# Optimization experiments

Measured on AMD Instinct MI355X. Metric: run time of the kernel, lower is better.

Reference implementation:

```python
import jax, jax.numpy as jnp
import numpy as np

M_NUMS = 4096
D_NUMS = 4096
PROJ = 256
EPS = 1e-10


def _lin(x, W, b):
    # torch nn.Linear: y = x @ W.T + b
    return x @ W.T + b


def setup_inputs() -> dict:
    key = jax.random.key(0)
    ks = jax.random.split(key, 16)
    N = M_NUMS + D_NUMS
    inp = {}
    inp["m_d_feat"] = jax.random.normal(ks[0], (N, PROJ), dtype=jnp.float32)
    inp["bigraph"] = jax.random.uniform(ks[1], (N, N), dtype=jnp.float32)
    # sparse-ish binary co-occurrence matrices (values !=0 / ==0 drive masks)
    inp["m_co"] = (jax.random.uniform(ks[2], (M_NUMS, M_NUMS)) < 0.1).astype(jnp.float32)
    inp["d_co"] = (jax.random.uniform(ks[3], (D_NUMS, D_NUMS)) < 0.1).astype(jnp.float32)
    # positive degrees in [1, 50) to keep 1/sqrt and 1/deg well-conditioned
    inp["m_co_deg"] = jax.random.uniform(ks[4], (M_NUMS, 2)) * 49.0 + 1.0
    inp["d_co_deg"] = jax.random.uniform(ks[5], (D_NUMS, 2)) * 49.0 + 1.0
    inp["m_d_degree"] = jax.random.uniform(ks[6], (M_NUMS,)) * 49.0 + 1.0
    inp["d_m_degree"] = jax.random.uniform(ks[7], (D_NUMS,)) * 49.0 + 1.0
    s = 0.02
    inp["Wm"] = jax.random.normal(ks[8], (3, PROJ, PROJ), dtype=jnp.float32) * s
    inp["bm"] = jnp.zeros((3, PROJ), dtype=jnp.float32)
    inp["Wd"] = jax.random.normal(ks[9], (3, PROJ, PROJ), dtype=jnp.float32) * s
    inp["bd"] = jnp.zeros((3, PROJ), dtype=jnp.float32)
    inp["Wx"] = jax.random.normal(ks[10], (8, PROJ, PROJ), dtype=jnp.float32) * s
    inp["bx"] = jnp.zeros((8, PROJ), dtype=jnp.float32)
    inp["central_m"] = jax.random.randint(ks[11], (M_NUMS,), 0, 2, dtype=jnp.int32)
    inp["central_d"] = jax.random.randint(ks[12], (D_NUMS,), 0, 2, dtype=jnp.int32)
    inp["m_nums"] = M_NUMS
    return inp


def _homog_block(feat, co, deg, W, b):
    # self-loop + degree-normalized co-occurrence / non-co-occurrence GEMMs
    n = feat.shape[0]
    diag = jnp.eye(n, dtype=bool)
    co_mask = (~diag) & (co != 0)
    non_mask = (~diag) & (co == 0)
    out = _lin(feat, W[0], b[0])  # self loop
    d0 = deg[:, 0]
    coeff0 = (1.0 / jnp.sqrt(d0[:, None] * d0[None, :] + EPS)) * co_mask.astype(feat.dtype)
    out = out + coeff0 @ _lin(feat, W[1], b[1])
    d1 = deg[:, 1]
    coeff1 = (1.0 / jnp.sqrt(d1[:, None] * d1[None, :] + EPS)) * non_mask.astype(feat.dtype)
    out = out + coeff1 @ _lin(feat, W[2], b[2])
    return out


def _cross_block(assoc, row_central, col_central, norm_row, src_feat, Wx, bx, pairs):
    # sum of 4 (central/normal x central/normal) masked-association GEMMs
    rc = row_central != 0
    cc = col_central != 0
    masks = [
        rc[:, None] & cc[None, :],
        rc[:, None] & (~cc)[None, :],
        (~rc)[:, None] & cc[None, :],
        (~rc)[:, None] & (~cc)[None, :],
    ]
    norm = (1.0 / norm_row)[:, None]
    out = jnp.zeros((assoc.shape[0], src_feat.shape[1]), dtype=src_feat.dtype)
    for mask, (i, j) in zip(masks, pairs):
        transformed = _lin(src_feat, Wx[i], bx[i]) + _lin(src_feat, Wx[j], bx[j])
        out = out + 0.5 * norm * ((assoc * mask.astype(assoc.dtype)) @ transformed)
    return out


def reference(m_d_feat, bigraph, m_co, m_co_deg, d_co, d_co_deg, m_d_degree,
              d_m_degree, Wm, bm, Wd, bd, Wx, bx, central_m, central_d, m_nums):
    m = m_nums
    m_feat = m_d_feat[:m]
    d_feat = m_d_feat[m:]

    out_m = _homog_block(m_feat, m_co, m_co_deg, Wm, bm)
    out_d = _homog_block(d_feat, d_co, d_co_deg, Wd, bd)

    # m <- d aggregation: Wx indices 0..7 =
    # [cm2cd, cd2cm, cm2nd, cd2nm, nm2cd, nd2cm, nm2nd, nd2nm]
    assoc_md = bigraph[:m, m:]
    out_m = out_m + _cross_block(assoc_md, central_m, central_d, m_d_degree,
                                 d_feat, Wx, bx,
                                 pairs=[(0, 1), (2, 5), (4, 3), (6, 7)])
    # d <- m aggregation (roles swapped)
    assoc_dm = bigraph[m:, :m]
    out_d = out_d + _cross_block(assoc_dm, central_d, central_m, d_m_degree,
                                 m_feat, Wx, bx,
                                 pairs=[(1, 0), (3, 4), (5, 2), (7, 6)])

    return jnp.concatenate([out_m, out_d], axis=0)
```

## Files before the change

kernel.cpp:

```cpp
#include <hip/hip_runtime.h>
#include <hip/hip_bf16.h>


typedef __bf16 bf16x8 __attribute__((ext_vector_type(8)));
typedef float floatx4 __attribute__((ext_vector_type(4)));
typedef float f32x4 __attribute__((ext_vector_type(4)));
using bf16 = __hip_bfloat16;

#define LDK 72

__device__ __forceinline__ float b2f(bf16 x){ return __bfloat162float(x); }
__device__ __forceinline__ bf16 f2b(float f){ return __float2bfloat16(f); }
__device__ __forceinline__ float rawb2f(unsigned short u){
  unsigned int x = ((unsigned int)u) << 16; float f; __builtin_memcpy(&f,&x,4); return f;
}
__device__ __forceinline__ unsigned short f2bu(float f){
  bf16 h = __float2bfloat16(f); unsigned short u; __builtin_memcpy(&u,&h,2); return u;
}
__device__ __forceinline__ uint4 cvt8(float4 a, float4 b){
  unsigned short u[8] = {f2bu(a.x),f2bu(a.y),f2bu(a.z),f2bu(a.w),
                         f2bu(b.x),f2bu(b.y),f2bu(b.z),f2bu(b.w)};
  uint4 v; __builtin_memcpy(&v,u,16); return v;
}
__device__ __forceinline__ void async_ld16(const void* gp, void* lp){
  typedef __attribute__((address_space(1))) const unsigned int GU;
  typedef __attribute__((address_space(3))) unsigned int LU;
  __builtin_amdgcn_global_load_lds((GU*)(unsigned long long)gp,
                                   (LU*)(unsigned int)(unsigned long long)lp,
                                   16, 0, 0);
}

__global__ void prep_kernel(const float* __restrict__ m_co_deg, const float* __restrict__ d_co_deg,
                            const float* __restrict__ m_d_degree, const float* __restrict__ d_m_degree,
                            const float* __restrict__ Wx, const float* __restrict__ bx,
                            float* __restrict__ scal, float* __restrict__ Sbuf, float* __restrict__ bSbuf)
{
  const int i = blockIdx.x*blockDim.x + threadIdx.x;
  if (i < 4096){
    scal[0*4096+i] = rsqrtf(m_co_deg[2*i]);
    scal[1*4096+i] = rsqrtf(m_co_deg[2*i+1]);
    scal[2*4096+i] = 0.5f / m_d_degree[i];
    scal[3*4096+i] = rsqrtf(d_co_deg[2*i]);
    scal[4*4096+i] = rsqrtf(d_co_deg[2*i+1]);
    scal[5*4096+i] = 0.5f / d_m_degree[i];
  }
  const int pa[4] = {0,2,3,6}, pb[4] = {1,5,4,7};
  if (i < 65536){
    #pragma unroll
    for (int s=0;s<4;s++)
      Sbuf[s*65536+i] = Wx[pa[s]*65536+i] + Wx[pb[s]*65536+i];
  }
  if (i < 256){
    #pragma unroll
    for (int s=0;s<4;s++)
      bSbuf[s*256+i] = bx[pa[s]*256+i] + bx[pb[s]*256+i];
  }
}

__global__ __launch_bounds__(256) void stage1_kernel(
    const float* __restrict__ feat, const float* __restrict__ Wm, const float* __restrict__ bm,
    const float* __restrict__ Wd, const float* __restrict__ bd,
    const float* __restrict__ Sbuf, const float* __restrict__ bSbuf, const float* __restrict__ scal,
    bf16* __restrict__ BHm, bf16* __restrict__ BHd,
    float* __restrict__ L0m, float* __restrict__ L0d,
    float* __restrict__ L2nm, float* __restrict__ L2nd,
    bf16* __restrict__ Tm, bf16* __restrict__ Td)
{
  __shared__ __align__(16) bf16 As[128*LDK];
  __shared__ __align__(16) bf16 Bs[128*LDK];
  const int p = blockIdx.y;
  const int side = p >> 3, widx = p & 7;
  const int bx_ = blockIdx.x;
  const bool modeT = (widx != 0 && widx != 7);
  const float* X = feat + (size_t)side*(4096*256);
  const float* Wb = side ? Wd : Wm;
  const float* W = (widx==0) ? Wb : (widx==7) ? (Wb + 2*65536)
                 : (widx<=2) ? (Wb + widx*65536) : (Sbuf + (widx-3)*65536);
  int rt, ct;
  if (!modeT){ rt = bx_>>1; ct = bx_&1; } else { rt = bx_&1; ct = bx_>>1; }
  const float* Amat = modeT ? W : X;
  const float* Bmat = modeT ? X : W;
  const int arow0 = rt*128, brow0 = ct*128;
  const int tid = threadIdx.x;
  const int lane = tid & 63, wv = tid>>6;
  const int wr = wv>>1, wc = wv&1, q = lane>>4, l15 = lane&15;

  floatx4 acc[4][4];
  #pragma unroll
  for (int i=0;i<4;i++)
    #pragma unroll
    for (int j=0;j<4;j++)
      #pragma unroll
      for (int r=0;r<4;r++) acc[i][j][r] = 0.f;

  for (int kt=0; kt<4; kt++){
    const int c0 = kt*64;
    __syncthreads();
    #pragma unroll
    for (int i=0;i<4;i++){
      const int id = tid + i*256;
      const int row = id>>3, kg = id&7;
      const float* ap = Amat + (size_t)(arow0+row)*256 + c0 + kg*8;
      const float* bp = Bmat + (size_t)(brow0+row)*256 + c0 + kg*8;
      float4 a0 = *(const float4*)ap, a1 = *(const float4*)(ap+4);
      float4 b0 = *(const float4*)bp, b1 = *(const float4*)(bp+4);
      *(uint4*)(&As[row*LDK + kg*8]) = cvt8(a0,a1);
      *(uint4*)(&Bs[row*LDK + kg*8]) = cvt8(b0,b1);
    }
    __syncthreads();
    #pragma unroll
    for (int ki=0; ki<2; ki++){
      bf16x8 af[4], bg[4];
      #pragma unroll
      for (int i=0;i<4;i++) af[i] = *(const bf16x8*)&As[(wr*64 + i*16 + l15)*LDK + ki*32 + q*8];
      #pragma unroll
      for (int j=0;j<4;j++) bg[j] = *(const bf16x8*)&Bs[(wc*64 + j*16 + l15)*LDK + ki*32 + q*8];
      #pragma unroll
      for (int i=0;i<4;i++)
        #pragma unroll
        for (int j=0;j<4;j++)
          acc[i][j] = __builtin_amdgcn_mfma_f32_16x16x32_bf16(af[i], bg[j], acc[i][j], 0,0,0);
    }
  }

  const float* bb = side ? bd : bm;
  const float* bias = (widx==0) ? bb : (widx==7) ? (bb + 512)
                    : (widx<=2) ? (bb + widx*256) : (bSbuf + (widx-3)*256);
  float* outF = nullptr; bf16* outB = nullptr; int pitch = 256; const float* scl = nullptr;
  if (widx==0){ outF = side? L0d : L0m; }
  else if (widx==7){ outF = side? L2nd : L2nm; }
  else if (widx==1){ outB = side? BHd : BHm; pitch = 4096; scl = scal + side*12288; }
  else if (widx==2){ outB = (side? BHd : BHm) + 256*4096; pitch = 4096; scl = scal + side*12288 + 4096; }
  else { outB = (side? Td : Tm) + (widx-3)*(256*4096); pitch = 4096; }

  #pragma unroll
  for (int i=0;i<4;i++){
    #pragma unroll
    for (int j=0;j<4;j++){
      const int gcol = brow0 + wc*64 + j*16 + l15;
      #pragma unroll
      for (int r=0;r<4;r++){
        const int grow = arow0 + wr*64 + i*16 + q*4 + r;
        float v = acc[i][j][r];
        const int nidx = modeT ? grow : gcol;
        v += bias[nidx];
        if (scl) v *= scl[gcol];
        if (outF) outF[(size_t)grow*pitch + gcol] = v;
        else      outB[(size_t)grow*pitch + gcol] = f2b(v);
      }
    }
  }
}

__global__ void stage2_kernel(const bf16* __restrict__ Tm, const bf16* __restrict__ Td,
                              const int* __restrict__ central_m, const int* __restrict__ central_d,
                              bf16* __restrict__ BXm, bf16* __restrict__ BXd)
{
  const int idx = blockIdx.x*blockDim.x + threadIdx.x;
  const int oside = idx >> 20;
  const int rem = idx & 1048575;
  const int n = rem >> 12;
  const int c = rem & 4095;
  const bf16* T = oside ? Tm : Td;
  const int* cen = oside ? central_m : central_d;
  bf16* B = oside ? BXd : BXm;
  const bool cc = cen[c] != 0;
  int v0i, v1i;
  if (!oside){ v0i = cc ? 2 : 3; v1i = cc ? 0 : 1; }
  else       { v0i = cc ? 1 : 3; v1i = cc ? 0 : 2; }
  const float v0 = b2f(T[(size_t)v0i*1048576 + (size_t)n*4096 + c]);
  const float v1 = b2f(T[(size_t)v1i*1048576 + (size_t)n*4096 + c]);
  B[(size_t)n*4096 + c]         = f2b(v0);
  B[(size_t)(256+n)*4096 + c]   = f2b(v1 - v0);
}

__global__ void colsum_kernel(const bf16* __restrict__ BHm, const bf16* __restrict__ BHd,
                              float* __restrict__ Scol)
{
  const int b = blockIdx.x;
  const int sd = b >> 8, n = b & 255;
  const int lane = threadIdx.x;
  const bf16* rowp = (sd ? BHd : BHm) + (size_t)(256+n)*4096;
  float s = 0.f;
  #pragma unroll
  for (int t=0;t<8;t++){
    const uint4 v = *(const uint4*)(rowp + t*512 + lane*8);
    unsigned short u[8]; __builtin_memcpy(u,&v,16);
    #pragma unroll
    for (int jj=0;jj<8;jj++) s += rawb2f(u[jj]);
  }
  #pragma unroll
  for (int off=32; off>0; off>>=1) s += __shfl_down(s, off);
  if (lane==0) Scol[sd*256 + n] = s;
}

__global__ __launch_bounds__(512,2) void gemm_kernel(
    const float* __restrict__ bigraph, const float* __restrict__ m_co, const float* __restrict__ d_co,
    const int* __restrict__ central_m, const int* __restrict__ central_d,
    const float* __restrict__ scal,
    const bf16* __restrict__ BHm, const bf16* __restrict__ BHd,
    const bf16* __restrict__ BXm, const bf16* __restrict__ BXd,
    float* __restrict__ partial)
{
  __shared__ __align__(16) bf16 As[2][128*32];
  __shared__ __align__(16) bf16 Bs[2][512*32];
  const int bid = blockIdx.x;
  const int w = (bid & 7)*32 + (bid >> 3);
  const int seg = w & 1, mt = (w >> 1) & 31, p = w >> 6;
  const int s = p & 1;
  const bool maskmode = (p < 2);
  const int k0 = seg*2048;
  const int rowbase = mt*128;
  const float* Asrc; int apitch; int acoff;
  if (p==0){ Asrc = m_co; apitch = 4096; acoff = 0; }
  else if (p==1){ Asrc = d_co; apitch = 4096; acoff = 0; }
  else if (p==2){ Asrc = bigraph; apitch = 8192; acoff = 4096; }
  else { Asrc = bigraph + (size_t)4096*8192; apitch = 8192; acoff = 0; }
  const bf16* B0 = (p==0) ? BHm : (p==1) ? BHd : (p==2) ? BXm : BXd;

  const int tid = threadIdx.x;
  const int lane = tid&63, wv = tid>>6;
  const int wr = wv>>2, wc = wv&3;
  const int q = lane>>4, l15 = lane&15;

  const int a_row = tid>>2, a_sg = tid&3;
  const int a_g  = a_sg ^ ((a_row>>1)&3);
  const int a_gr = rowbase + a_row;
  const float* a_base = Asrc + (size_t)a_gr*apitch + acoff + a_g*8;
  int b_roff[4]; int b_ldsoff[4];
  #pragma unroll
  for (int j=0;j<4;j++){
    const int cb = wv*256 + j*64;
    const int chunk = cb + lane;
    const int row = chunk>>2, sg = chunk&3;
    const int gg = sg ^ ((row>>1)&3);
    b_roff[j] = row*4096 + gg*8;
    b_ldsoff[j] = cb*8;
  }

  floatx4 acc0[4][4], acc1[4][4];
  #pragma unroll
  for (int i=0;i<4;i++)
    #pragma unroll
    for (int j=0;j<4;j++)
      #pragma unroll
      for (int r=0;r<4;r++){ acc0[i][j][r] = 0.f; acc1[i][j][r] = 0.f; }

  auto issueB = [&](int kkg, int buf){
    #pragma unroll
    for (int j=0;j<4;j++)
      async_ld16(B0 + (size_t)b_roff[j] + kkg, &Bs[buf][b_ldsoff[j]]);
  };
  auto writeA = [&](f32x4 a0, f32x4 a1, int kkg, int buf){
    const float av[8] = {a0[0],a0[1],a0[2],a0[3],a1[0],a1[1],a1[2],a1[3]};
    unsigned short u[8];
    if (maskmode){
      const int cbase = kkg + a_g*8;
      #pragma unroll
      for (int jj=0;jj<8;jj++)
        u[jj] = (av[jj]!=0.0f && (cbase+jj)!=a_gr) ? (unsigned short)0x3F80 : (unsigned short)0;
    } else {
      #pragma unroll
      for (int jj=0;jj<8;jj++) u[jj] = f2bu(av[jj]);
    }
    uint4 w4; __builtin_memcpy(&w4,u,16);
    *(uint4*)(&As[buf][tid*8]) = w4;
  };

  {
    const int kkg = k0;
    const float* ap = a_base + kkg;
    f32x4 a0 = __builtin_nontemporal_load((const f32x4*)ap);
    f32x4 a1 = __builtin_nontemporal_load((const f32x4*)(ap+4));
    issueB(kkg, 0);
    writeA(a0, a1, kkg, 0);
  }
  __syncthreads();

  for (int kt=0; kt<64; kt++){
    const int cur = kt & 1;
    const bool pre = (kt+1 < 64);
    f32x4 a0, a1;
    const int nkkg = k0 + (kt+1)*32;
    if (pre){
      const float* ap = a_base + nkkg;
      a0 = __builtin_nontemporal_load((const f32x4*)ap);
      a1 = __builtin_nontemporal_load((const f32x4*)(ap+4));
      issueB(nkkg, cur^1);
    }
    __builtin_amdgcn_sched_barrier(0);

    bf16x8 af[4];
    #pragma unroll
    for (int i=0;i<4;i++){
      const int ra = wr*64 + i*16 + l15;
      af[i] = *(const bf16x8*)&As[cur][ra*32 + ((q ^ ((ra>>1)&3)))*8];
    }
    #pragma unroll
    for (int j=0;j<4;j++){
      const int rb = wc*64 + j*16 + l15;
      const int off = rb*32 + ((q ^ ((rb>>1)&3)))*8;
      const bf16x8 b0 = *(const bf16x8*)&Bs[cur][off];
      const bf16x8 b1 = *(const bf16x8*)&Bs[cur][256*32 + off];
      #pragma unroll
      for (int i=0;i<4;i++){
        acc0[i][j] = __builtin_amdgcn_mfma_f32_16x16x32_bf16(af[i], b0, acc0[i][j], 0,0,0);
        acc1[i][j] = __builtin_amdgcn_mfma_f32_16x16x32_bf16(af[i], b1, acc1[i][j], 0,0,0);
      }
    }
    __builtin_amdgcn_sched_barrier(0);

    if (pre) writeA(a0, a1, nkkg, cur^1);
    __syncthreads();
  }

  const float* scS = scal + (size_t)s*12288;
  const int* cenR = s ? central_d : central_m;
  float* pb = partial + ((size_t)seg*4 + p)*4096*256;
  #pragma unroll
  for (int i=0;i<4;i++){
    #pragma unroll
    for (int r_=0;r_<4;r_++){
      const int rl = rowbase + wr*64 + i*16 + q*4 + r_;
      float w0, w1;
      if (maskmode){ w0 = scS[rl]; w1 = -scS[4096+rl]; }
      else { const float nr = scS[8192+rl]; w0 = nr; w1 = cenR[rl] ? nr : 0.f; }
      #pragma unroll
      for (int j=0;j<4;j++){
        const int gcol = wc*64 + j*16 + l15;
        pb[(size_t)rl*256 + gcol] = w0*acc0[i][j][r_] + w1*acc1[i][j][r_];
      }
    }
  }
}

__global__ void reduce_kernel(const float* __restrict__ partial,
                              const float* __restrict__ L0m, const float* __restrict__ L0d,
                              const float* __restrict__ L2nm, const float* __restrict__ L2nd,
                              const float* __restrict__ Scol, const float* __restrict__ scal,
                              float* __restrict__ out)
{
  const int idx = blockIdx.x*blockDim.x + threadIdx.x;
  const int r = idx >> 6;
  const int n4 = (idx & 63) << 2;
  const int s = r >> 12;
  const int rl = r & 4095;
  const float r1 = scal[s*12288 + 4096 + rl];
  const size_t rb = (size_t)rl*256 + n4;
  const float4 l0 = *(const float4*)((s? L0d : L0m) + rb);
  const float4 l2 = *(const float4*)((s? L2nd : L2nm) + rb);
  const float4 sc = *(const float4*)(Scol + s*256 + n4);
  const float4 h0 = *(const float4*)(partial + (size_t)(0*4+s)*1048576 + rb);
  const float4 h1 = *(const float4*)(partial + (size_t)(1*4+s)*1048576 + rb);
  const float4 x0 = *(const float4*)(partial + (size_t)(0*4+2+s)*1048576 + rb);
  const float4 x1 = *(const float4*)(partial + (size_t)(1*4+2+s)*1048576 + rb);
  const float r1sq = r1*r1;
  float4 o;
  o.x = l0.x + h0.x+h1.x + x0.x+x1.x + r1*sc.x - r1sq*l2.x;
  o.y = l0.y + h0.y+h1.y + x0.y+x1.y + r1*sc.y - r1sq*l2.y;
  o.z = l0.z + h0.z+h1.z + x0.z+x1.z + r1*sc.z - r1sq*l2.z;
  o.w = l0.w + h0.w+h1.w + x0.w+x1.w + r1*sc.w - r1sq*l2.w;
  *(float4*)(out + (size_t)r*256 + n4) = o;
}

extern "C" void kernel_launch(void* const* d_in, const int* in_sizes, int n_in,
                              void* d_out, int out_size, void* d_ws, size_t ws_size,
                              hipStream_t stream)
{
  (void)in_sizes; (void)n_in; (void)out_size; (void)ws_size;
  const float* m_d_feat   = (const float*)d_in[0];
  const float* bigraph    = (const float*)d_in[1];
  const float* m_co       = (const float*)d_in[2];
  const float* d_co       = (const float*)d_in[3];
  const float* m_co_deg   = (const float*)d_in[4];
  const float* d_co_deg   = (const float*)d_in[5];
  const float* m_d_degree = (const float*)d_in[6];
  const float* d_m_degree = (const float*)d_in[7];
  const float* Wm = (const float*)d_in[8];
  const float* bm = (const float*)d_in[9];
  const float* Wd = (const float*)d_in[10];
  const float* bd = (const float*)d_in[11];
  const float* Wx = (const float*)d_in[12];
  const float* bx = (const float*)d_in[13];
  const int* central_m = (const int*)d_in[14];
  const int* central_d = (const int*)d_in[15];

  char* ws = (char*)d_ws;
  bf16*  BHm  = (bf16*) (ws + 0);
  bf16*  BHd  = (bf16*) (ws + 4194304);
  bf16*  BXm  = (bf16*) (ws + 8388608);
  bf16*  BXd  = (bf16*) (ws + 12582912);
  float* L0m  = (float*)(ws + 16777216);
  float* L0d  = (float*)(ws + 20971520);
  float* L2nm = (float*)(ws + 25165824);
  float* L2nd = (float*)(ws + 29360128);
  float* Sbuf = (float*)(ws + 33554432);
  float* bSbuf= (float*)(ws + 34603008);
  float* scal = (float*)(ws + 34607104);
  float* Scol = (float*)(ws + 34705408);
  bf16*  Tm   = (bf16*) (ws + 34707456);
  bf16*  Td   = (bf16*) (ws + 43096064);
  float* partial = (float*)(ws + 34707456);

  prep_kernel<<<256, 256, 0, stream>>>(m_co_deg, d_co_deg, m_d_degree, d_m_degree,
                                       Wx, bx, scal, Sbuf, bSbuf);
  stage1_kernel<<<dim3(64,16), 256, 0, stream>>>(m_d_feat, Wm, bm, Wd, bd, Sbuf, bSbuf, scal,
                                                 BHm, BHd, L0m, L0d, L2nm, L2nd, Tm, Td);
  stage2_kernel<<<8192, 256, 0, stream>>>(Tm, Td, central_m, central_d, BXm, BXd);
  colsum_kernel<<<512, 64, 0, stream>>>(BHm, BHd, Scol);
  gemm_kernel<<<256, 512, 0, stream>>>(bigraph, m_co, d_co, central_m, central_d,
                                       scal, BHm, BHd, BXm, BXd, partial);
  reduce_kernel<<<2048, 256, 0, stream>>>(partial, L0m, L0d, L2nm, L2nd, Scol, scal, (float*)d_out);
}
```

Measured before the change: 569.2 us.

## Triple-buffer B tiles with two-stage prefetch and manual waitcnt barriers

Grows the shared-memory B staging buffer from two to three slots and issues async B loads two K-steps ahead instead of one, so global-to-LDS latency has more time to hide behind MFMA work. `__syncthreads` is replaced by explicit `s_waitcnt lgkmcnt` plus `s_barrier`. B loads still in flight are left outstanding, and ordering relies on the vmcnt wait the compiler inserts for the A register loads. Fragment LDS offsets are precomputed outside the loop. The larger LDS footprint (about 112KB per block) likely no longer allows two blocks per CU, which the launch bounds assume, so occupancy may drop.

```diff
diff --git a/kernel.cpp b/kernel.cpp
--- a/kernel.cpp
+++ b/kernel.cpp
@@ -203,7 +203,7 @@
     float* __restrict__ partial)
 {
   __shared__ __align__(16) bf16 As[2][128*32];
-  __shared__ __align__(16) bf16 Bs[2][512*32];
+  __shared__ __align__(16) bf16 Bs[3][512*32];
   const int bid = blockIdx.x;
   const int w = (bid & 7)*32 + (bid >> 3);
   const int seg = w & 1, mt = (w >> 1) & 31, p = w >> 6;
@@ -237,6 +237,17 @@
     b_roff[j] = row*4096 + gg*8;
     b_ldsoff[j] = cb*8;
   }
+  int af_off[4], bf_off[4];
+  #pragma unroll
+  for (int i=0;i<4;i++){
+    const int ra = wr*64 + i*16 + l15;
+    af_off[i] = ra*32 + ((q ^ ((ra>>1)&3)))*8;
+  }
+  #pragma unroll
+  for (int j=0;j<4;j++){
+    const int rb = wc*64 + j*16 + l15;
+    bf_off[j] = rb*32 + ((q ^ ((rb>>1)&3)))*8;
+  }
 
   floatx4 acc0[4][4], acc1[4][4];
   #pragma unroll
@@ -268,50 +279,59 @@
   };
 
   {
-    const int kkg = k0;
-    const float* ap = a_base + kkg;
+    const float* ap = a_base + k0;
     f32x4 a0 = __builtin_nontemporal_load((const f32x4*)ap);
     f32x4 a1 = __builtin_nontemporal_load((const f32x4*)(ap+4));
-    issueB(kkg, 0);
-    writeA(a0, a1, kkg, 0);
-  }
-  __syncthreads();
-
+    __builtin_amdgcn_sched_barrier(0);
+    issueB(k0, 0);
+    issueB(k0 + 32, 1);
+    __builtin_amdgcn_sched_barrier(0);
+    writeA(a0, a1, k0, 0);
+    asm volatile("s_waitcnt vmcnt(4) lgkmcnt(0)" ::: "memory");
+    __builtin_amdgcn_s_barrier();
+    __builtin_amdgcn_sched_barrier(0);
+  }
+
+  int bcur = 0;
   for (int kt=0; kt<64; kt++){
-    const int cur = kt & 1;
-    const bool pre = (kt+1 < 64);
+    const int curA = kt & 1;
+    const bool pre1 = (kt+1 < 64);
+    const bool pre2 = (kt+2 < 64);
     f32x4 a0, a1;
-    const int nkkg = k0 + (kt+1)*32;
-    if (pre){
-      const float* ap = a_base + nkkg;
+    if (pre1){
+      const float* ap = a_base + k0 + (kt+1)*32;
       a0 = __builtin_nontemporal_load((const f32x4*)ap);
       a1 = __builtin_nontemporal_load((const f32x4*)(ap+4));
-      issueB(nkkg, cur^1);
-    }
-    __builtin_amdgcn_sched_barrier(0);
-
-    bf16x8 af[4];
-    #pragma unroll
-    for (int i=0;i<4;i++){
-      const int ra = wr*64 + i*16 + l15;
-      af[i] = *(const bf16x8*)&As[cur][ra*32 + ((q ^ ((ra>>1)&3)))*8];
-    }
-    #pragma unroll
-    for (int j=0;j<4;j++){
-      const int rb = wc*64 + j*16 + l15;
-      const int off = rb*32 + ((q ^ ((rb>>1)&3)))*8;
-      const bf16x8 b0 = *(const bf16x8*)&Bs[cur][off];
-      const bf16x8 b1 = *(const bf16x8*)&Bs[cur][256*32 + off];
-      #pragma unroll
-      for (int i=0;i<4;i++){
-        acc0[i][j] = __builtin_amdgcn_mfma_f32_16x16x32_bf16(af[i], b0, acc0[i][j], 0,0,0);
-        acc1[i][j] = __builtin_amdgcn_mfma_f32_16x16x32_bf16(af[i], b1, acc1[i][j], 0,0,0);
+    }
+    __builtin_amdgcn_sched_barrier(0);
+    if (pre2){
+      const int bw = (bcur+2 < 3) ? bcur+2 : bcur-1;
+      issueB(k0 + (kt+2)*32, bw);
+    }
+    __builtin_amdgcn_sched_barrier(0);
+    {
+      const bf16* AsC = &As[curA][0];
+      const bf16* BsC = &Bs[bcur][0];
+      bf16x8 af[4];
+      #pragma unroll
+      for (int i=0;i<4;i++) af[i] = *(const bf16x8*)&AsC[af_off[i]];
+      #pragma unroll
+      for (int j=0;j<4;j++){
+        const bf16x8 b0 = *(const bf16x8*)&BsC[bf_off[j]];
+        const bf16x8 b1 = *(const bf16x8*)&BsC[256*32 + bf_off[j]];
+        #pragma unroll
+        for (int i=0;i<4;i++){
+          acc0[i][j] = __builtin_amdgcn_mfma_f32_16x16x32_bf16(af[i], b0, acc0[i][j], 0,0,0);
+          acc1[i][j] = __builtin_amdgcn_mfma_f32_16x16x32_bf16(af[i], b1, acc1[i][j], 0,0,0);
+        }
       }
     }
     __builtin_amdgcn_sched_barrier(0);
-
-    if (pre) writeA(a0, a1, nkkg, cur^1);
-    __syncthreads();
+    if (pre1) writeA(a0, a1, k0 + (kt+1)*32, curA^1);
+    asm volatile("s_waitcnt lgkmcnt(0)" ::: "memory");
+    __builtin_amdgcn_s_barrier();
+    __builtin_amdgcn_sched_barrier(0);
+    bcur = (bcur+1 < 3) ? bcur+1 : 0;
   }
 
   const float* scS = scal + (size_t)s*12288;
```

Result: faster. 548.8 us (-3.6%).
